# Kernel tuning notes

Hardware: AMD Instinct MI355X
Metric: run time of the kernel (lower is better)

The kernel has to match this reference:

```python
import jax, jax.numpy as jnp
import numpy as np

B, S, H, NH = 4, 1024, 2048, 16
D = H // NH  # head_dim = 128


def setup_inputs() -> dict:
    key = jax.random.key(0)
    ks = jax.random.split(key, 10)
    # RoPE tables: angle[t, j] = t * 10000^(-2j/D), cos/sin of the complex freqs_cis
    t = jnp.arange(S, dtype=jnp.float32)
    inv_freq = 1.0 / (10000.0 ** (jnp.arange(0, D, 2, dtype=jnp.float32) / D))
    ang = t[:, None] * inv_freq[None, :]  # [S, D//2]
    w = 0.02
    return {
        "hidden_states": jax.random.normal(ks[0], (B, S, H), jnp.float32),
        "freqs_cos": jnp.cos(ang),
        "freqs_sin": jnp.sin(ang),
        "attention_mask": jnp.ones((B, 1, 1, S), jnp.float32),
        "Wq": jax.random.normal(ks[1], (H, H), jnp.float32) * w,
        "bq": jnp.zeros((H,), jnp.float32),
        "Wk": jax.random.normal(ks[2], (H, H), jnp.float32) * w,
        "bk": jnp.zeros((H,), jnp.float32),
        "Wv": jax.random.normal(ks[3], (H, H), jnp.float32) * w,
        "bv": jnp.zeros((H,), jnp.float32),
        "Wo": jax.random.normal(ks[4], (H, H), jnp.float32) * w,
        "bo": jnp.zeros((H,), jnp.float32),
    }


def _rope(x, cos, sin):
    # x: [B, S, NH, D]; cos/sin: [S, D//2]. Complex multiply on (even, odd) pairs.
    x2 = x.reshape(x.shape[:-1] + (D // 2, 2))
    x0, x1 = x2[..., 0], x2[..., 1]
    c = cos[None, :, None, :]
    s = sin[None, :, None, :]
    o0 = x0 * c - x1 * s
    o1 = x0 * s + x1 * c
    return jnp.stack([o0, o1], axis=-1).reshape(x.shape)


def reference(hidden_states, freqs_cos, freqs_sin, attention_mask,
              Wq, bq, Wk, bk, Wv, bv, Wo, bo):
    b, s, _ = hidden_states.shape
    q = (hidden_states @ Wq.T + bq).reshape(b, s, NH, D)
    k = (hidden_states @ Wk.T + bk).reshape(b, s, NH, D)
    v = (hidden_states @ Wv.T + bv).reshape(b, s, NH, D)
    q = _rope(q, freqs_cos, freqs_sin)
    k = _rope(k, freqs_cos, freqs_sin)
    # scores: [b, h, q, k]; original scales by sqrt(embed_dim)=sqrt(hidden_size)
    scores = jnp.einsum('bqhd,bkhd->bhqk', q, k) / jnp.sqrt(jnp.float32(H))
    scores = jnp.where(attention_mask == 0, jnp.float32(-1e9), scores)
    probs = jax.nn.softmax(scores, axis=-1)  # dropout is identity in eval
    ctx = jnp.einsum('bhqk,bkhd->bqhd', probs, v).reshape(b, s, H)
    return ctx @ Wo.T + bo
```

## Files before the change

kernel.cpp:

```cpp
#include <hip/hip_runtime.h>
#include <stdint.h>

#define BATCH 4
#define SEQ   1024
#define NHEAD 16
#define DHEAD 128
#define HDIM  2048
#define GM    4096
#define GN    2048
#define GK    2048

typedef __attribute__((ext_vector_type(8))) short short8;
typedef __attribute__((ext_vector_type(4))) float f32x4;

__device__ __forceinline__ uint16_t f2bf(float f) {
  uint32_t u = __builtin_bit_cast(uint32_t, f);
  u += 0x7fffu + ((u >> 16) & 1u);
  return (uint16_t)(u >> 16);
}
__device__ __forceinline__ float bf2f(uint16_t h) {
  return __builtin_bit_cast(float, (uint32_t)h << 16);
}

__device__ __forceinline__ uint32_t swz128(uint32_t a) { return a ^ (((a >> 7) & 7u) << 4); }
__device__ __forceinline__ uint32_t swz256(uint32_t a) { return a ^ (((a >> 8) & 7u) << 4); }

#define GAS __attribute__((address_space(1)))
#define LAS __attribute__((address_space(3)))
__device__ __forceinline__ void gload_lds16(const void* g, void* l) {
  __builtin_amdgcn_global_load_lds((GAS const void*)g, (LAS void*)l, 16, 0, 0);
}

__global__ void cvt_kernel(const float* __restrict__ in, uint16_t* __restrict__ out, int n8) {
  int i = blockIdx.x * 256 + threadIdx.x;
  if (i >= n8) return;
  const float4* p = (const float4*)in + (size_t)i * 2;
  float4 a = p[0], b = p[1];
  uint32_t w0 = f2bf(a.x) | ((uint32_t)f2bf(a.y) << 16);
  uint32_t w1 = f2bf(a.z) | ((uint32_t)f2bf(a.w) << 16);
  uint32_t w2 = f2bf(b.x) | ((uint32_t)f2bf(b.y) << 16);
  uint32_t w3 = f2bf(b.z) | ((uint32_t)f2bf(b.w) << 16);
  int4 r; r.x = (int)w0; r.y = (int)w1; r.z = (int)w2; r.w = (int)w3;
  *(int4*)(out + (size_t)i * 8) = r;
}

__global__ void cvtw_kernel(const float* __restrict__ W0, const float* __restrict__ W1,
                            const float* __restrict__ W2, const float* __restrict__ W3,
                            uint16_t* __restrict__ out) {
  const float* src = (blockIdx.y == 0) ? W0 : (blockIdx.y == 1) ? W1 : (blockIdx.y == 2) ? W2 : W3;
  int i = blockIdx.x * 256 + threadIdx.x;
  const float4* p = (const float4*)src + (size_t)i * 2;
  float4 a = p[0], b = p[1];
  uint32_t w0 = f2bf(a.x) | ((uint32_t)f2bf(a.y) << 16);
  uint32_t w1 = f2bf(a.z) | ((uint32_t)f2bf(a.w) << 16);
  uint32_t w2 = f2bf(b.x) | ((uint32_t)f2bf(b.y) << 16);
  uint32_t w3 = f2bf(b.z) | ((uint32_t)f2bf(b.w) << 16);
  int4 r; r.x = (int)w0; r.y = (int)w1; r.z = (int)w2; r.w = (int)w3;
  *(int4*)(out + (size_t)blockIdx.y * HDIM * HDIM + (size_t)i * 8) = r;
}

__global__ void rope_kernel(uint16_t* __restrict__ qb, uint16_t* __restrict__ kb,
                            const float* __restrict__ fcos, const float* __restrict__ fsin) {
  uint32_t i = blockIdx.x * 256 + threadIdx.x;
  uint16_t* p = (blockIdx.y == 0 ? qb : kb) + (size_t)i * 8;
  uint32_t e0 = i * 8;
  uint32_t row = e0 >> 11;
  uint32_t col = e0 & 2047;
  uint32_t s = row & (SEQ - 1);
  uint32_t pi = (col & (DHEAD - 1)) >> 1;
  float4 cv = *(const float4*)(fcos + (size_t)s * 64 + pi);
  float4 sv = *(const float4*)(fsin + (size_t)s * 64 + pi);
  int4 raw = *(const int4*)p;
  uint16_t u[8]; *(int4*)u = raw;
  float cc[4] = {cv.x, cv.y, cv.z, cv.w}, ss[4] = {sv.x, sv.y, sv.z, sv.w};
#pragma unroll
  for (int t = 0; t < 4; ++t) {
    float x0 = bf2f(u[2 * t]), x1 = bf2f(u[2 * t + 1]);
    float o0 = x0 * cc[t] - x1 * ss[t];
    float o1 = x0 * ss[t] + x1 * cc[t];
    u[2 * t] = f2bf(o0); u[2 * t + 1] = f2bf(o1);
  }
  *(int4*)p = *(int4*)u;
}

template <int MODE>
__device__ __forceinline__ void gemm_body(const uint16_t* __restrict__ A,
                                          const uint16_t* __restrict__ Bw,
                                          const float* __restrict__ bias,
                                          void* __restrict__ Cout) {
  __shared__ __align__(16) char smA[128 * 128];
  __shared__ __align__(16) char smB[128 * 128];
  const int tid = threadIdx.x, lane = tid & 63, wid = tid >> 6;
  const int c = lane & 15, g = lane >> 4;
  const int row0 = blockIdx.x * 128, col0 = blockIdx.y * 128;
  const int wr = wid >> 1, wc = wid & 1;
  f32x4 acc[4][4] = {};
  const uint32_t oBase = wid * 4096 + lane * 16;

  for (int kk = 0; kk < GK; kk += 64) {
#pragma unroll
    for (int q = 0; q < 4; ++q) {
      uint32_t o = oBase + q * 1024;
      uint32_t r = o >> 7;
      uint32_t cb = (o & 127) ^ ((r & 7u) << 4);
      gload_lds16((const char*)A + ((size_t)(row0 + r) * GK + kk) * 2 + cb,
                  smA + wid * 4096 + q * 1024);
      gload_lds16((const char*)Bw + ((size_t)(col0 + r) * GK + kk) * 2 + cb,
                  smB + wid * 4096 + q * 1024);
    }
    __syncthreads();
    short8 af[4][2], bf[4][2];
#pragma unroll
    for (int m = 0; m < 4; ++m) {
      const uint32_t row = (uint32_t)(wr * 64 + m * 16 + c);
#pragma unroll
      for (int ks = 0; ks < 2; ++ks)
        af[m][ks] = *(const short8*)(smA + row * 128 + (((uint32_t)(ks * 64 + g * 16)) ^ ((row & 7u) << 4)));
    }
#pragma unroll
    for (int n = 0; n < 4; ++n) {
      const uint32_t row = (uint32_t)(wc * 64 + n * 16 + c);
#pragma unroll
      for (int ks = 0; ks < 2; ++ks)
        bf[n][ks] = *(const short8*)(smB + row * 128 + (((uint32_t)(ks * 64 + g * 16)) ^ ((row & 7u) << 4)));
    }
#pragma unroll
    for (int m = 0; m < 4; ++m)
#pragma unroll
      for (int n = 0; n < 4; ++n)
#pragma unroll
        for (int ks = 0; ks < 2; ++ks)
          acc[m][n] = __builtin_amdgcn_mfma_f32_16x16x32_bf16(af[m][ks], bf[n][ks], acc[m][n], 0, 0, 0);
    __syncthreads();
  }

  float bn[4];
#pragma unroll
  for (int n = 0; n < 4; ++n) bn[n] = bias[col0 + wc * 64 + n * 16 + c];
#pragma unroll
  for (int m = 0; m < 4; ++m) {
    const int gr = row0 + wr * 64 + m * 16 + g * 4;
#pragma unroll
    for (int n = 0; n < 4; ++n) {
      const int gc = col0 + wc * 64 + n * 16 + c;
#pragma unroll
      for (int jj = 0; jj < 4; ++jj) {
        float v = acc[m][n][jj] + bn[n];
        if (MODE == 1) ((float*)Cout)[(size_t)(gr + jj) * GN + gc] = v;
        else           ((uint16_t*)Cout)[(size_t)(gr + jj) * GN + gc] = f2bf(v);
      }
    }
  }
}

__global__ __launch_bounds__(256, 2) void gemm_qkv_kernel(
    const uint16_t* __restrict__ X,
    const uint16_t* __restrict__ Wq, const uint16_t* __restrict__ Wk, const uint16_t* __restrict__ Wv,
    const float* __restrict__ bq, const float* __restrict__ bk, const float* __restrict__ bv,
    uint16_t* __restrict__ qo, uint16_t* __restrict__ ko, uint16_t* __restrict__ vo) {
  const uint16_t* W; const float* bias; uint16_t* out;
  if (blockIdx.z == 0)      { W = Wq; bias = bq; out = qo; }
  else if (blockIdx.z == 1) { W = Wk; bias = bk; out = ko; }
  else                      { W = Wv; bias = bv; out = vo; }
  gemm_body<0>(X, W, bias, out);
}

__global__ __launch_bounds__(256, 2) void gemm_out_kernel(
    const uint16_t* __restrict__ ctx, const uint16_t* __restrict__ Wo,
    const float* __restrict__ bo, float* __restrict__ out) {
  gemm_body<1>(ctx, Wo, bo, out);
}

__global__ __launch_bounds__(256, 2) void attn_kernel(
    const uint16_t* __restrict__ q, const uint16_t* __restrict__ k,
    const uint16_t* __restrict__ v, const float* __restrict__ mask,
    uint16_t* __restrict__ ctx) {
  __shared__ __align__(16) char smK[64 * 256];
  __shared__ __align__(16) char smVT[128 * 128];
  __shared__ __align__(16) char smP[64 * 128];
  __shared__ float smMask[64];
  __shared__ float smScale[64];

  const int tid = threadIdx.x, lane = tid & 63, wid = tid >> 6;
  const int c = lane & 15, g = lane >> 4;
  const int b = blockIdx.z, h = blockIdx.y, q0 = blockIdx.x * 64;
  const float scale = 0.022097086912079608f;

  short8 qreg[4];
  {
    const uint16_t* qrow = q + (size_t)(b * SEQ + q0 + wid * 16 + c) * HDIM + h * DHEAD;
#pragma unroll
    for (int ks = 0; ks < 4; ++ks) qreg[ks] = *(const short8*)(qrow + ks * 32 + g * 8);
  }

  const int kvg = tid >> 5;
  const int d0  = (tid & 31) * 4;

  float mreg = -1e30f, lreg = 0.f;
  f32x4 oacc[8] = {};

  for (int t = 0; t < 16; ++t) {
    const int kv0 = t * 64;
    __syncthreads();
#pragma unroll
    for (int i = 0; i < 4; ++i) {
      uint32_t o = wid * 4096 + i * 1024 + lane * 16;
      uint32_t r = o >> 8;
      uint32_t cb = swz256(o) & 255;
      gload_lds16((const char*)k + ((size_t)(b * SEQ + kv0 + r) * HDIM + h * DHEAD) * 2 + cb,
                  smK + wid * 4096 + i * 1024);
    }
    if (tid < 64) smMask[tid] = mask[b * SEQ + kv0 + tid];
    {
      const uint16_t* vsrc = v + (size_t)(b * SEQ + kv0 + kvg * 8) * HDIM + h * DHEAD + d0;
      uint32_t vw[8][2];
#pragma unroll
      for (int e = 0; e < 8; ++e) {
        uint2 t2 = *(const uint2*)(vsrc + (size_t)e * HDIM);
        vw[e][0] = t2.x; vw[e][1] = t2.y;
      }
#pragma unroll
      for (int j = 0; j < 4; ++j) {
        const int hw = j >> 1, sh = (j & 1) * 16;
        int4 pk;
        pk.x = (int)(((vw[0][hw] >> sh) & 0xffffu) | (((vw[1][hw] >> sh) & 0xffffu) << 16));
        pk.y = (int)(((vw[2][hw] >> sh) & 0xffffu) | (((vw[3][hw] >> sh) & 0xffffu) << 16));
        pk.z = (int)(((vw[4][hw] >> sh) & 0xffffu) | (((vw[5][hw] >> sh) & 0xffffu) << 16));
        pk.w = (int)(((vw[6][hw] >> sh) & 0xffffu) | (((vw[7][hw] >> sh) & 0xffffu) << 16));
        *(int4*)(smVT + swz128((uint32_t)((d0 + j) * 128 + kvg * 16))) = pk;
      }
    }
    __syncthreads();

    f32x4 st[4] = {};
#pragma unroll
    for (int ks = 0; ks < 4; ++ks) {
#pragma unroll
      for (int mi = 0; mi < 4; ++mi) {
        short8 kf = *(const short8*)(smK + swz256((uint32_t)((mi * 16 + c) * 256 + ks * 64 + g * 16)));
        st[mi] = __builtin_amdgcn_mfma_f32_16x16x32_bf16(kf, qreg[ks], st[mi], 0, 0, 0);
      }
    }
    float sv[4][4];
    float pmax = -1e30f;
#pragma unroll
    for (int mi = 0; mi < 4; ++mi) {
      float4 mb = *(const float4*)(smMask + mi * 16 + g * 4);
      float mbv[4] = {mb.x, mb.y, mb.z, mb.w};
#pragma unroll
      for (int jj = 0; jj < 4; ++jj) {
        float s = st[mi][jj] * scale;
        if (mbv[jj] == 0.f) s = -1e9f;
        sv[mi][jj] = s;
        pmax = fmaxf(pmax, s);
      }
    }
    pmax = fmaxf(pmax, __shfl_xor(pmax, 16, 64));
    pmax = fmaxf(pmax, __shfl_xor(pmax, 32, 64));
    float mnew = fmaxf(mreg, pmax);
    float fac = __expf(mreg - mnew);
    float rsum = 0.f;
    uint32_t pw[4][2];
#pragma unroll
    for (int mi = 0; mi < 4; ++mi) {
      float p0 = __expf(sv[mi][0] - mnew);
      float p1 = __expf(sv[mi][1] - mnew);
      float p2 = __expf(sv[mi][2] - mnew);
      float p3 = __expf(sv[mi][3] - mnew);
      rsum += (p0 + p1) + (p2 + p3);
      pw[mi][0] = f2bf(p0) | ((uint32_t)f2bf(p1) << 16);
      pw[mi][1] = f2bf(p2) | ((uint32_t)f2bf(p3) << 16);
    }
    rsum += __shfl_xor(rsum, 16, 64);
    rsum += __shfl_xor(rsum, 32, 64);
    lreg = lreg * fac + rsum;
    mreg = mnew;
#pragma unroll
    for (int mi = 0; mi < 4; ++mi) {
      uint32_t addr = swz128((uint32_t)((wid * 16 + c) * 128 + (mi * 16 + g * 4) * 2));
      uint2 wv; wv.x = pw[mi][0]; wv.y = pw[mi][1];
      *(uint2*)(smP + addr) = wv;
    }
    if (g == 0) smScale[wid * 16 + c] = fac;
    __syncthreads();

    float4 fv = *(const float4*)(smScale + wid * 16 + g * 4);
    float fvv[4] = {fv.x, fv.y, fv.z, fv.w};
#pragma unroll
    for (int nj = 0; nj < 8; ++nj)
#pragma unroll
      for (int jj = 0; jj < 4; ++jj) oacc[nj][jj] *= fvv[jj];
#pragma unroll
    for (int ks = 0; ks < 2; ++ks) {
      short8 pf = *(const short8*)(smP + swz128((uint32_t)((wid * 16 + c) * 128 + ks * 64 + g * 16)));
#pragma unroll
      for (int nj = 0; nj < 8; ++nj) {
        short8 vf = *(const short8*)(smVT + swz128((uint32_t)((nj * 16 + c) * 128 + ks * 64 + g * 16)));
        oacc[nj] = __builtin_amdgcn_mfma_f32_16x16x32_bf16(pf, vf, oacc[nj], 0, 0, 0);
      }
    }
  }

  __syncthreads();
  if (g == 0) smScale[wid * 16 + c] = lreg;
  __syncthreads();
  float4 lv = *(const float4*)(smScale + wid * 16 + g * 4);
  float inv[4] = {1.f / lv.x, 1.f / lv.y, 1.f / lv.z, 1.f / lv.w};
#pragma unroll
  for (int nj = 0; nj < 8; ++nj) {
#pragma unroll
    for (int jj = 0; jj < 4; ++jj) {
      int qrow = q0 + wid * 16 + g * 4 + jj;
      int dcol = h * DHEAD + nj * 16 + c;
      ctx[(size_t)(b * SEQ + qrow) * HDIM + dcol] = f2bf(oacc[nj][jj] * inv[jj]);
    }
  }
}

extern "C" void kernel_launch(void* const* d_in, const int* in_sizes, int n_in,
                              void* d_out, int out_size, void* d_ws, size_t ws_size,
                              hipStream_t stream) {
  const float* hs   = (const float*)d_in[0];
  const float* fcos = (const float*)d_in[1];
  const float* fsin = (const float*)d_in[2];
  const float* mask = (const float*)d_in[3];
  const float* Wq = (const float*)d_in[4];  const float* bq = (const float*)d_in[5];
  const float* Wk = (const float*)d_in[6];  const float* bk = (const float*)d_in[7];
  const float* Wv = (const float*)d_in[8];  const float* bv = (const float*)d_in[9];
  const float* Wo = (const float*)d_in[10]; const float* bo = (const float*)d_in[11];
  float* out = (float*)d_out;

  char* ws = (char*)d_ws;
  const size_t XB = (size_t)GM * HDIM * 2;
  const size_t WB = (size_t)HDIM * HDIM * 2;
  uint16_t* Xbf = (uint16_t*)(ws);
  uint16_t* Wqb = (uint16_t*)(ws + XB);
  uint16_t* Wkb = (uint16_t*)(ws + XB + WB);
  uint16_t* Wvb = (uint16_t*)(ws + XB + 2 * WB);
  uint16_t* Wob = (uint16_t*)(ws + XB + 3 * WB);
  uint16_t* qb  = (uint16_t*)(ws + XB + 4 * WB);
  uint16_t* kb  = (uint16_t*)(ws + XB + 4 * WB + XB);
  uint16_t* vb  = (uint16_t*)(ws + XB + 4 * WB + 2 * XB);

  cvt_kernel<<<4096, 256, 0, stream>>>(hs, Xbf, (GM * HDIM) / 8);
  cvtw_kernel<<<dim3(2048, 4), 256, 0, stream>>>(Wq, Wk, Wv, Wo, Wqb);

  gemm_qkv_kernel<<<dim3(GM / 128, GN / 128, 3), 256, 0, stream>>>(
      Xbf, Wqb, Wkb, Wvb, bq, bk, bv, qb, kb, vb);

  rope_kernel<<<dim3((GM * HDIM) / 8 / 256, 2, 1), 256, 0, stream>>>(qb, kb, fcos, fsin);

  attn_kernel<<<dim3(SEQ / 64, NHEAD, BATCH), 256, 0, stream>>>(qb, kb, vb, mask, Xbf);

  gemm_out_kernel<<<dim3(GM / 128, GN / 128, 1), 256, 0, stream>>>(Xbf, Wob, bo, out);
}
```

Before: 280.0 us.

## Rewrite attention with 32x32 MFMA, register-resident P and lazy rescaling

The attention kernel moves from 16x16x32 to 32x32x16 bf16 MFMA with 128-query tiles (32 rows per wave), halving the block count and remapping block indices for locality. P is kept in registers via cross-lane shuffles instead of going through LDS, which drops the P buffer and one barrier per KV tile. The online-softmax rescale is skipped unless the running max grows by more than 8, and bf16 packing uses the hardware cvt_pk instruction. The output is staged through LDS so ctx is written with wide coalesced stores; in exchange the kernel uses more registers and has fewer blocks for occupancy.

```diff
diff --git a/kernel.cpp b/kernel.cpp
--- a/kernel.cpp
+++ b/kernel.cpp
@@ -10,8 +10,10 @@
 #define GN    2048
 #define GK    2048
 
-typedef __attribute__((ext_vector_type(8))) short short8;
-typedef __attribute__((ext_vector_type(4))) float f32x4;
+typedef __attribute__((ext_vector_type(8)))  short    short8;
+typedef __attribute__((ext_vector_type(4)))  float    f32x4;
+typedef __attribute__((ext_vector_type(16))) float    f32x16;
+typedef __attribute__((ext_vector_type(4)))  uint32_t u32x4;
 
 __device__ __forceinline__ uint16_t f2bf(float f) {
   uint32_t u = __builtin_bit_cast(uint32_t, f);
@@ -20,6 +22,11 @@
 }
 __device__ __forceinline__ float bf2f(uint16_t h) {
   return __builtin_bit_cast(float, (uint32_t)h << 16);
+}
+__device__ __forceinline__ uint32_t cvtpk(float lo, float hi) {
+  uint32_t r;
+  asm("v_cvt_pk_bf16_f32 %0, %1, %2" : "=v"(r) : "v"(lo), "v"(hi));
+  return r;
 }
 
 __device__ __forceinline__ uint32_t swz128(uint32_t a) { return a ^ (((a >> 7) & 7u) << 4); }
@@ -175,44 +182,47 @@
     const uint16_t* __restrict__ q, const uint16_t* __restrict__ k,
     const uint16_t* __restrict__ v, const float* __restrict__ mask,
     uint16_t* __restrict__ ctx) {
-  __shared__ __align__(16) char smK[64 * 256];
-  __shared__ __align__(16) char smVT[128 * 128];
-  __shared__ __align__(16) char smP[64 * 128];
-  __shared__ float smMask[64];
-  __shared__ float smScale[64];
+  __shared__ __align__(16) char pool[33024];
+  char* smK  = pool;
+  char* smVT = pool + 16384;
+  float* smMaskF = (float*)(pool + 32768);
+  float* smT = (float*)pool;
 
   const int tid = threadIdx.x, lane = tid & 63, wid = tid >> 6;
-  const int c = lane & 15, g = lane >> 4;
-  const int b = blockIdx.z, h = blockIdx.y, q0 = blockIdx.x * 64;
+  const int c32 = lane & 31, hi = lane >> 5;
+  const int lb = (blockIdx.x & 7) * 64 + (blockIdx.x >> 3);
+  const int qt = lb & 7, bh = lb >> 3;
+  const int h = bh & (NHEAD - 1), b = bh >> 4;
+  const int q0 = qt * 128;
   const float scale = 0.022097086912079608f;
 
-  short8 qreg[4];
+  short8 qreg[8];
   {
-    const uint16_t* qrow = q + (size_t)(b * SEQ + q0 + wid * 16 + c) * HDIM + h * DHEAD;
-#pragma unroll
-    for (int ks = 0; ks < 4; ++ks) qreg[ks] = *(const short8*)(qrow + ks * 32 + g * 8);
+    const uint16_t* qrow = q + (size_t)(b * SEQ + q0 + wid * 32 + c32) * HDIM + h * DHEAD;
+#pragma unroll
+    for (int ks = 0; ks < 8; ++ks) qreg[ks] = *(const short8*)(qrow + ks * 16 + hi * 8);
   }
 
   const int kvg = tid >> 5;
-  const int d0  = (tid & 31) * 4;
+  const int d0v = (tid & 31) * 4;
 
   float mreg = -1e30f, lreg = 0.f;
-  f32x4 oacc[8] = {};
+  f32x16 o[4] = {};
 
   for (int t = 0; t < 16; ++t) {
     const int kv0 = t * 64;
     __syncthreads();
 #pragma unroll
     for (int i = 0; i < 4; ++i) {
-      uint32_t o = wid * 4096 + i * 1024 + lane * 16;
-      uint32_t r = o >> 8;
-      uint32_t cb = swz256(o) & 255;
+      uint32_t o_ = wid * 4096 + i * 1024 + lane * 16;
+      uint32_t r = o_ >> 8;
+      uint32_t cb = swz256(o_) & 255;
       gload_lds16((const char*)k + ((size_t)(b * SEQ + kv0 + r) * HDIM + h * DHEAD) * 2 + cb,
                   smK + wid * 4096 + i * 1024);
     }
-    if (tid < 64) smMask[tid] = mask[b * SEQ + kv0 + tid];
+    if (tid < 64) smMaskF[tid] = mask[b * SEQ + kv0 + tid];
     {
-      const uint16_t* vsrc = v + (size_t)(b * SEQ + kv0 + kvg * 8) * HDIM + h * DHEAD + d0;
+      const uint16_t* vsrc = v + (size_t)(b * SEQ + kv0 + kvg * 8) * HDIM + h * DHEAD + d0v;
       uint32_t vw[8][2];
 #pragma unroll
       for (int e = 0; e < 8; ++e) {
@@ -227,93 +237,120 @@
         pk.y = (int)(((vw[2][hw] >> sh) & 0xffffu) | (((vw[3][hw] >> sh) & 0xffffu) << 16));
         pk.z = (int)(((vw[4][hw] >> sh) & 0xffffu) | (((vw[5][hw] >> sh) & 0xffffu) << 16));
         pk.w = (int)(((vw[6][hw] >> sh) & 0xffffu) | (((vw[7][hw] >> sh) & 0xffffu) << 16));
-        *(int4*)(smVT + swz128((uint32_t)((d0 + j) * 128 + kvg * 16))) = pk;
-      }
-    }
-    __syncthreads();
-
-    f32x4 st[4] = {};
-#pragma unroll
-    for (int ks = 0; ks < 4; ++ks) {
-#pragma unroll
-      for (int mi = 0; mi < 4; ++mi) {
-        short8 kf = *(const short8*)(smK + swz256((uint32_t)((mi * 16 + c) * 256 + ks * 64 + g * 16)));
-        st[mi] = __builtin_amdgcn_mfma_f32_16x16x32_bf16(kf, qreg[ks], st[mi], 0, 0, 0);
-      }
-    }
-    float sv[4][4];
+        *(int4*)(smVT + swz128((uint32_t)((d0v + j) * 128 + kvg * 16))) = pk;
+      }
+    }
+    __syncthreads();
+
+    f32x16 st[2] = {};
+#pragma unroll
+    for (int ks = 0; ks < 8; ++ks) {
+#pragma unroll
+      for (int mi = 0; mi < 2; ++mi) {
+        const uint32_t row = (uint32_t)(mi * 32 + c32);
+        short8 kf = *(const short8*)(smK + row * 256 +
+                    (((uint32_t)(ks * 32 + hi * 16)) ^ ((row & 7u) << 4)));
+        st[mi] = __builtin_amdgcn_mfma_f32_32x32x16_bf16(kf, qreg[ks], st[mi], 0, 0, 0);
+      }
+    }
+
+    float p[32];
     float pmax = -1e30f;
 #pragma unroll
-    for (int mi = 0; mi < 4; ++mi) {
-      float4 mb = *(const float4*)(smMask + mi * 16 + g * 4);
-      float mbv[4] = {mb.x, mb.y, mb.z, mb.w};
-#pragma unroll
-      for (int jj = 0; jj < 4; ++jj) {
-        float s = st[mi][jj] * scale;
-        if (mbv[jj] == 0.f) s = -1e9f;
-        sv[mi][jj] = s;
+    for (int mi = 0; mi < 2; ++mi) {
+      const float* mb = smMaskF + mi * 32 + hi * 4;
+      float4 m0 = *(const float4*)(mb);
+      float4 m1 = *(const float4*)(mb + 8);
+      float4 m2 = *(const float4*)(mb + 16);
+      float4 m3 = *(const float4*)(mb + 24);
+      float mm[16] = {m0.x, m0.y, m0.z, m0.w, m1.x, m1.y, m1.z, m1.w,
+                      m2.x, m2.y, m2.z, m2.w, m3.x, m3.y, m3.z, m3.w};
+#pragma unroll
+      for (int r = 0; r < 16; ++r) {
+        float s = st[mi][r] * scale;
+        if (mm[r] == 0.f) s = -1e9f;
+        p[mi * 16 + r] = s;
         pmax = fmaxf(pmax, s);
       }
     }
-    pmax = fmaxf(pmax, __shfl_xor(pmax, 16, 64));
     pmax = fmaxf(pmax, __shfl_xor(pmax, 32, 64));
-    float mnew = fmaxf(mreg, pmax);
-    float fac = __expf(mreg - mnew);
+
+    if (!__all(pmax <= mreg + 8.f)) {
+      float mnew = fmaxf(mreg, pmax);
+      float fac = __expf(mreg - mnew);
+      lreg *= fac;
+#pragma unroll
+      for (int dt = 0; dt < 4; ++dt)
+#pragma unroll
+        for (int e = 0; e < 16; ++e) o[dt][e] *= fac;
+      mreg = mnew;
+    }
+
     float rsum = 0.f;
-    uint32_t pw[4][2];
-#pragma unroll
-    for (int mi = 0; mi < 4; ++mi) {
-      float p0 = __expf(sv[mi][0] - mnew);
-      float p1 = __expf(sv[mi][1] - mnew);
-      float p2 = __expf(sv[mi][2] - mnew);
-      float p3 = __expf(sv[mi][3] - mnew);
-      rsum += (p0 + p1) + (p2 + p3);
-      pw[mi][0] = f2bf(p0) | ((uint32_t)f2bf(p1) << 16);
-      pw[mi][1] = f2bf(p2) | ((uint32_t)f2bf(p3) << 16);
-    }
-    rsum += __shfl_xor(rsum, 16, 64);
+    short8 pfrag[4];
+#pragma unroll
+    for (int mi = 0; mi < 2; ++mi) {
+      float pe[16];
+#pragma unroll
+      for (int r = 0; r < 16; ++r) {
+        pe[r] = __expf(p[mi * 16 + r] - mreg);
+        rsum += pe[r];
+      }
+      uint32_t w[8], s[8];
+#pragma unroll
+      for (int j = 0; j < 8; ++j) w[j] = cvtpk(pe[2 * j], pe[2 * j + 1]);
+#pragma unroll
+      for (int j = 0; j < 8; ++j) s[j] = (uint32_t)__shfl_xor((int)w[j], 32, 64);
+      u32x4 f0, f1;
+      f0[0] = hi ? s[2] : w[0];  f0[1] = hi ? s[3] : w[1];
+      f0[2] = hi ? w[2] : s[0];  f0[3] = hi ? w[3] : s[1];
+      f1[0] = hi ? s[6] : w[4];  f1[1] = hi ? s[7] : w[5];
+      f1[2] = hi ? w[6] : s[4];  f1[3] = hi ? w[7] : s[5];
+      pfrag[mi * 2]     = __builtin_bit_cast(short8, f0);
+      pfrag[mi * 2 + 1] = __builtin_bit_cast(short8, f1);
+    }
     rsum += __shfl_xor(rsum, 32, 64);
-    lreg = lreg * fac + rsum;
-    mreg = mnew;
-#pragma unroll
-    for (int mi = 0; mi < 4; ++mi) {
-      uint32_t addr = swz128((uint32_t)((wid * 16 + c) * 128 + (mi * 16 + g * 4) * 2));
-      uint2 wv; wv.x = pw[mi][0]; wv.y = pw[mi][1];
-      *(uint2*)(smP + addr) = wv;
-    }
-    if (g == 0) smScale[wid * 16 + c] = fac;
-    __syncthreads();
-
-    float4 fv = *(const float4*)(smScale + wid * 16 + g * 4);
-    float fvv[4] = {fv.x, fv.y, fv.z, fv.w};
-#pragma unroll
-    for (int nj = 0; nj < 8; ++nj)
-#pragma unroll
-      for (int jj = 0; jj < 4; ++jj) oacc[nj][jj] *= fvv[jj];
-#pragma unroll
-    for (int ks = 0; ks < 2; ++ks) {
-      short8 pf = *(const short8*)(smP + swz128((uint32_t)((wid * 16 + c) * 128 + ks * 64 + g * 16)));
-#pragma unroll
-      for (int nj = 0; nj < 8; ++nj) {
-        short8 vf = *(const short8*)(smVT + swz128((uint32_t)((nj * 16 + c) * 128 + ks * 64 + g * 16)));
-        oacc[nj] = __builtin_amdgcn_mfma_f32_16x16x32_bf16(pf, vf, oacc[nj], 0, 0, 0);
-      }
-    }
-  }
-
-  __syncthreads();
-  if (g == 0) smScale[wid * 16 + c] = lreg;
-  __syncthreads();
-  float4 lv = *(const float4*)(smScale + wid * 16 + g * 4);
-  float inv[4] = {1.f / lv.x, 1.f / lv.y, 1.f / lv.z, 1.f / lv.w};
-#pragma unroll
-  for (int nj = 0; nj < 8; ++nj) {
-#pragma unroll
-    for (int jj = 0; jj < 4; ++jj) {
-      int qrow = q0 + wid * 16 + g * 4 + jj;
-      int dcol = h * DHEAD + nj * 16 + c;
-      ctx[(size_t)(b * SEQ + qrow) * HDIM + dcol] = f2bf(oacc[nj][jj] * inv[jj]);
-    }
+    lreg += rsum;
+
+#pragma unroll
+    for (int dt = 0; dt < 4; ++dt) {
+      const uint32_t row = (uint32_t)(dt * 32 + c32);
+#pragma unroll
+      for (int e = 0; e < 4; ++e) {
+        short8 vf = *(const short8*)(smVT + row * 128 +
+                    (((uint32_t)(e * 32 + hi * 16)) ^ ((row & 7u) << 4)));
+        o[dt] = __builtin_amdgcn_mfma_f32_32x32x16_bf16(vf, pfrag[e], o[dt], 0, 0, 0);
+      }
+    }
+  }
+
+  const float linv = 1.f / lreg;
+  float* myT = smT + wid * (32 * 36);
+  const int qe = lane >> 1, de0 = (lane & 1) * 16;
+#pragma unroll
+  for (int dt = 0; dt < 4; ++dt) {
+    __syncthreads();
+#pragma unroll
+    for (int r = 0; r < 16; ++r) {
+      const int drow = (r & 3) + 8 * (r >> 2) + 4 * hi;
+      myT[c32 * 36 + drow] = o[dt][r] * linv;
+    }
+    asm volatile("s_waitcnt lgkmcnt(0)" ::: "memory");
+    float vv[16];
+#pragma unroll
+    for (int j = 0; j < 4; ++j) {
+      float4 rd = *(const float4*)(myT + qe * 36 + de0 + j * 4);
+      vv[j * 4 + 0] = rd.x; vv[j * 4 + 1] = rd.y; vv[j * 4 + 2] = rd.z; vv[j * 4 + 3] = rd.w;
+    }
+    uint32_t pw[8];
+#pragma unroll
+    for (int m = 0; m < 8; ++m)
+      pw[m] = f2bf(vv[2 * m]) | ((uint32_t)f2bf(vv[2 * m + 1]) << 16);
+    uint16_t* dst = ctx + (size_t)(b * SEQ + q0 + wid * 32 + qe) * HDIM + h * DHEAD + dt * 32 + de0;
+    int4 s0; s0.x = (int)pw[0]; s0.y = (int)pw[1]; s0.z = (int)pw[2]; s0.w = (int)pw[3];
+    int4 s1; s1.x = (int)pw[4]; s1.y = (int)pw[5]; s1.z = (int)pw[6]; s1.w = (int)pw[7];
+    *(int4*)(dst) = s0;
+    *(int4*)(dst + 8) = s1;
   }
 }
 
@@ -350,7 +387,7 @@
 
   rope_kernel<<<dim3((GM * HDIM) / 8 / 256, 2, 1), 256, 0, stream>>>(qb, kb, fcos, fsin);
 
-  attn_kernel<<<dim3(SEQ / 64, NHEAD, BATCH), 256, 0, stream>>>(qb, kb, vb, mask, Xbf);
+  attn_kernel<<<512, 256, 0, stream>>>(qb, kb, vb, mask, Xbf);
 
   gemm_out_kernel<<<dim3(GM / 128, GN / 128, 1), 256, 0, stream>>>(Xbf, Wob, bo, out);
 }
```

After: 243.3 us. 1.15x faster.
